# Kernel tuning notes

Measured on AMD Instinct MI355X. Metric: run time of the kernel, lower is better.

Reference implementation:

```python
import math
import jax, jax.numpy as jnp
import numpy as np

NUM_HEADS = 12
KEEP_RATE = 0.7


def setup_inputs() -> dict:
    key = jax.random.key(0)
    k1, k2, k3 = jax.random.split(key, 3)
    B, N, C = 16, 577, 768
    x = jax.random.normal(k1, (B, N, C), dtype=jnp.float32)
    qkv_w = jax.random.normal(k2, (3 * C, C), dtype=jnp.float32) * 0.02
    proj_w = jax.random.normal(k3, (C, C), dtype=jnp.float32) * 0.02
    proj_b = jnp.zeros((C,), dtype=jnp.float32)
    return {"x": x, "qkv_w": qkv_w, "proj_w": proj_w, "proj_b": proj_b}


def reference(x, qkv_w, proj_w, proj_b):
    B, N, C = x.shape
    H = NUM_HEADS
    hd = C // H
    scale = hd ** -0.5
    # qkv projection (no bias): [B, N, 3C] -> [3, B, H, N, hd]
    qkv = (x @ qkv_w.T).reshape(B, N, 3, H, hd).transpose(2, 0, 3, 1, 4)
    q, k, v = qkv[0], qkv[1], qkv[2]
    attn = jax.nn.softmax(jnp.einsum('bhnd,bhmd->bhnm', q, k) * scale, axis=-1)
    out = jnp.einsum('bhnm,bhmd->bhnd', attn, v)          # [B,H,N,hd]
    out = out.transpose(0, 2, 1, 3).reshape(B, N, C)
    out = out @ proj_w.T + proj_b
    # CLS-token attention pruning (keep_rate < 1.0, return_idx=True path)
    left_tokens = math.ceil(KEEP_RATE * (N - 1))
    cls_attn = attn[:, :, 0, 1:].mean(axis=1)             # [B, N-1], mean over heads
    _, idx = jax.lax.top_k(cls_attn, left_tokens)         # sorted descending
    index = jnp.broadcast_to(idx[:, :, None], (B, left_tokens, C))
    return out, idx, index, cls_attn
```

## Files before the change

### kernel.cpp

```cpp
#include <hip/hip_runtime.h>
#include <math.h>

#define BB 16
#define NN 577
#define CC 768
#define HH 12
#define HD 64
#define MM (BB*NN)
#define MPAD 9344
#define LEFT 404
#define NPAD 608
#define NQT 10

typedef __attribute__((ext_vector_type(8))) short short8v;
typedef __attribute__((ext_vector_type(4))) float f32x4;

__device__ __forceinline__ unsigned short f2bf(float f) {
    union { float f; unsigned int u; } v; v.f = f;
    unsigned int r = v.u + 0x7fffu + ((v.u >> 16) & 1u);
    return (unsigned short)(r >> 16);
}

__global__ __launch_bounds__(256) void k_qv_fused(const float* __restrict__ X,
                                                  const float* __restrict__ W,
                                                  float* __restrict__ kb,
                                                  unsigned short* __restrict__ kbh,
                                                  const unsigned short* __restrict__ xbh,
                                                  const unsigned short* __restrict__ wqkv,
                                                  unsigned short* __restrict__ qbh,
                                                  unsigned short* __restrict__ Vt)
{
    __shared__ __align__(16) char smem[16384];
    const int bid = blockIdx.x;
    const int t = threadIdx.x;

    if (bid % 3 == 0) {
        const int kidx = bid / 3;
        float (*Xs)[128] = (float(*)[128])smem;
        float (*Ws)[128] = (float(*)[128])(smem + 8192);
        const int tx = t & 15, ty = t >> 4;
        const int m0 = (kidx % 73) * 128;
        const int n0 = 768 + (kidx / 73) * 128;
        const int sm = t & 127;
        const int sk = (t >> 7) * 8;

        float acc[8][8];
        #pragma unroll
        for (int i = 0; i < 8; ++i)
            #pragma unroll
            for (int j = 0; j < 8; ++j) acc[i][j] = 0.f;

        const int gm = m0 + sm;
        const float* px = X + (size_t)gm * CC + sk;
        const float* pw = W + (size_t)(n0 + sm) * CC + sk;

        float4 a0 = make_float4(0.f,0.f,0.f,0.f), a1 = a0, b0, b1;
        if (gm < MM) { a0 = *(const float4*)px; a1 = *(const float4*)(px + 4); }
        b0 = *(const float4*)pw; b1 = *(const float4*)(pw + 4);

        for (int kk = 0; kk < CC; kk += 16) {
            Xs[sk+0][sm] = a0.x; Xs[sk+1][sm] = a0.y; Xs[sk+2][sm] = a0.z; Xs[sk+3][sm] = a0.w;
            Xs[sk+4][sm] = a1.x; Xs[sk+5][sm] = a1.y; Xs[sk+6][sm] = a1.z; Xs[sk+7][sm] = a1.w;
            Ws[sk+0][sm] = b0.x; Ws[sk+1][sm] = b0.y; Ws[sk+2][sm] = b0.z; Ws[sk+3][sm] = b0.w;
            Ws[sk+4][sm] = b1.x; Ws[sk+5][sm] = b1.y; Ws[sk+6][sm] = b1.z; Ws[sk+7][sm] = b1.w;
            __syncthreads();
            if (kk + 16 < CC) {
                a0 = make_float4(0.f,0.f,0.f,0.f); a1 = a0;
                if (gm < MM) { a0 = *(const float4*)(px + kk + 16); a1 = *(const float4*)(px + kk + 20); }
                b0 = *(const float4*)(pw + kk + 16); b1 = *(const float4*)(pw + kk + 20);
            }
            #pragma unroll
            for (int k = 0; k < 16; ++k) {
                float a[8], bv[8];
                *(float4*)&a[0]  = *(const float4*)&Xs[k][ty*4];
                *(float4*)&a[4]  = *(const float4*)&Xs[k][64 + ty*4];
                *(float4*)&bv[0] = *(const float4*)&Ws[k][tx*4];
                *(float4*)&bv[4] = *(const float4*)&Ws[k][64 + tx*4];
                #pragma unroll
                for (int i = 0; i < 8; ++i)
                    #pragma unroll
                    for (int j = 0; j < 8; ++j)
                        acc[i][j] = fmaf(a[i], bv[j], acc[i][j]);
            }
            __syncthreads();
        }
        #pragma unroll
        for (int i = 0; i < 8; ++i) {
            const int mrow = m0 + ((i < 4) ? (ty*4 + i) : (64 + ty*4 + i - 4));
            if (mrow >= MM) continue;
            const int b_ = mrow / NN;
            const int n_ = mrow - b_ * NN;
            #pragma unroll
            for (int j = 0; j < 8; ++j) {
                const int col = (n0 - 768) + ((j < 4) ? (tx*4 + j) : (64 + tx*4 + j - 4));
                const int h = col >> 6, d = col & 63;
                const float a = acc[i][j];
                kb [(((size_t)b_ * HH + h) * NN   + n_) * HD + d] = a;
                kbh[(((size_t)b_ * HH + h) * NPAD + n_) * HD + d] = f2bf(a);
            }
        }
    } else {
        const int qbid = (bid / 3) * 2 + (bid % 3) - 1;
        unsigned short* As = (unsigned short*)smem;
        unsigned short* Bs = (unsigned short*)(smem + 8192);
        const int w = t >> 6, l = t & 63;
        const int l15 = l & 15, lk = l >> 4;
        const int wm = w >> 1, wn = w & 1;
        const int m0 = (qbid % 73) * 128;
        const int by = qbid / 73;
        const int isV = by >= 6;
        const int nlocal0 = (isV ? (by - 6) : by) * 128;
        const int wrow0 = (isV ? 1536 : 0) + nlocal0;
        const int r0 = t >> 2, segp = t & 3;

        f32x4 acc[4][4];
        #pragma unroll
        for (int i = 0; i < 4; ++i)
            #pragma unroll
            for (int j = 0; j < 4; ++j) acc[i][j] = (f32x4){0.f,0.f,0.f,0.f};

        const unsigned short* ga = xbh  + (size_t)(m0 + r0) * CC + segp * 8;
        const unsigned short* gb = wqkv + (size_t)(wrow0 + r0) * CC + segp * 8;

        for (int kk = 0; kk < CC; kk += 32) {
            const short8v a0 = *(const short8v*)(ga + kk);
            const short8v a1 = *(const short8v*)(ga + kk + (size_t)64 * CC);
            const short8v b0 = *(const short8v*)(gb + kk);
            const short8v b1 = *(const short8v*)(gb + kk + (size_t)64 * CC);
            __syncthreads();
            *(short8v*)&As[(r0)      * 32 + segp*8] = a0;
            *(short8v*)&As[(64 + r0) * 32 + segp*8] = a1;
            *(short8v*)&Bs[(r0)      * 32 + segp*8] = b0;
            *(short8v*)&Bs[(64 + r0) * 32 + segp*8] = b1;
            __syncthreads();
            short8v fa[4], fb[4];
            #pragma unroll
            for (int i = 0; i < 4; ++i) fa[i] = *(const short8v*)&As[(wm*64 + i*16 + l15)*32 + lk*8];
            #pragma unroll
            for (int j = 0; j < 4; ++j) fb[j] = *(const short8v*)&Bs[(wn*64 + j*16 + l15)*32 + lk*8];
            #pragma unroll
            for (int i = 0; i < 4; ++i)
                #pragma unroll
                for (int j = 0; j < 4; ++j)
                    acc[i][j] = __builtin_amdgcn_mfma_f32_16x16x32_bf16(fa[i], fb[j], acc[i][j], 0, 0, 0);
        }

        const int nb = nlocal0 + wn*64 + l15;
        #pragma unroll
        for (int i = 0; i < 4; ++i) {
            #pragma unroll
            for (int r = 0; r < 4; ++r) {
                const int m = m0 + wm*64 + i*16 + 4*lk + r;
                if (m >= MM) continue;
                const int b_ = m / NN, tok = m - b_ * NN;
                #pragma unroll
                for (int j = 0; j < 4; ++j) {
                    const int nl = nb + j*16;
                    const int h = nl >> 6, d = nl & 63;
                    const unsigned short v = f2bf(acc[i][j][r]);
                    if (isV) Vt [(((size_t)b_*HH + h)*HD + d)*NPAD + tok] = v;
                    else     qbh[(((size_t)b_*HH + h)*NPAD + tok)*HD + d] = v;
                }
            }
        }
    }
}

__global__ __launch_bounds__(256) void qcls_kernel(const float* __restrict__ X,
                                                   const float* __restrict__ W,
                                                   float* __restrict__ qcls)
{
    const int b = blockIdx.x;
    const int col = blockIdx.y * 256 + threadIdx.x;
    const float* xr = X + (size_t)b * NN * CC;
    const float* wr = W + (size_t)col * CC;
    float acc = 0.f;
    for (int k = 0; k < CC; ++k) acc = fmaf(xr[k], wr[k], acc);
    qcls[(size_t)b * CC + col] = acc;
}

#define N4X 1772544
#define N4W 442368
#define N4P 147456
__global__ __launch_bounds__(256) void convert3(const float* __restrict__ x,
                                                const float* __restrict__ wq,
                                                const float* __restrict__ wp,
                                                unsigned short* __restrict__ xb,
                                                unsigned short* __restrict__ wqb,
                                                unsigned short* __restrict__ wpb)
{
    int g = blockIdx.x * 256 + threadIdx.x;
    const float* src; unsigned short* dst;
    if (g < N4X)            { src = x;  dst = xb;  }
    else if (g < N4X + N4W) { g -= N4X; src = wq; dst = wqb; }
    else                    { g -= (N4X + N4W); src = wp; dst = wpb; }
    const float4 v = ((const float4*)src)[g];
    ushort4 o;
    o.x = f2bf(v.x); o.y = f2bf(v.y); o.z = f2bf(v.z); o.w = f2bf(v.w);
    ((ushort4*)dst)[g] = o;
}

__global__ __launch_bounds__(256) void proj_mfma(const unsigned short* __restrict__ aobh,
                                                 const unsigned short* __restrict__ wpb,
                                                 const float* __restrict__ bias,
                                                 float* __restrict__ outp)
{
    __shared__ unsigned short As[128*32];
    __shared__ unsigned short Bs[128*32];
    const int t = threadIdx.x;
    const int w = t >> 6, l = t & 63;
    const int l15 = l & 15, lk = l >> 4;
    const int wm = w >> 1, wn = w & 1;
    const int m0 = blockIdx.x * 128;
    const int n0 = blockIdx.y * 128;
    const int r0 = t >> 2, segp = t & 3;

    f32x4 acc[4][4];
    #pragma unroll
    for (int i = 0; i < 4; ++i)
        #pragma unroll
        for (int j = 0; j < 4; ++j) acc[i][j] = (f32x4){0.f,0.f,0.f,0.f};

    const unsigned short* ga = aobh + (size_t)(m0 + r0) * CC + segp * 8;
    const unsigned short* gb = wpb  + (size_t)(n0 + r0) * CC + segp * 8;

    for (int kk = 0; kk < CC; kk += 32) {
        const short8v a0 = *(const short8v*)(ga + kk);
        const short8v a1 = *(const short8v*)(ga + kk + (size_t)64 * CC);
        const short8v b0 = *(const short8v*)(gb + kk);
        const short8v b1 = *(const short8v*)(gb + kk + (size_t)64 * CC);
        __syncthreads();
        *(short8v*)&As[(r0)      * 32 + segp*8] = a0;
        *(short8v*)&As[(64 + r0) * 32 + segp*8] = a1;
        *(short8v*)&Bs[(r0)      * 32 + segp*8] = b0;
        *(short8v*)&Bs[(64 + r0) * 32 + segp*8] = b1;
        __syncthreads();
        short8v fa[4], fb[4];
        #pragma unroll
        for (int i = 0; i < 4; ++i) fa[i] = *(const short8v*)&As[(wm*64 + i*16 + l15)*32 + lk*8];
        #pragma unroll
        for (int j = 0; j < 4; ++j) fb[j] = *(const short8v*)&Bs[(wn*64 + j*16 + l15)*32 + lk*8];
        #pragma unroll
        for (int i = 0; i < 4; ++i)
            #pragma unroll
            for (int j = 0; j < 4; ++j)
                acc[i][j] = __builtin_amdgcn_mfma_f32_16x16x32_bf16(fa[i], fb[j], acc[i][j], 0, 0, 0);
    }

    const int nb = n0 + wn*64 + l15;
    #pragma unroll
    for (int i = 0; i < 4; ++i) {
        #pragma unroll
        for (int r = 0; r < 4; ++r) {
            const int m = m0 + wm*64 + i*16 + 4*lk + r;
            if (m >= MM) continue;
            #pragma unroll
            for (int j = 0; j < 4; ++j) {
                const int n = nb + j*16;
                outp[(size_t)m * CC + n] = acc[i][j][r] + bias[n];
            }
        }
    }
}

__global__ __launch_bounds__(256) void attn_mfma(const unsigned short* __restrict__ qbh,
                                                 const unsigned short* __restrict__ kbh,
                                                 const unsigned short* __restrict__ Vt,
                                                 unsigned short* __restrict__ aobh)
{
    __shared__ __align__(16) unsigned short plds[4][16][32];
    const int bid = blockIdx.x;
    const int bh  = bid / NQT;
    const int qt  = bid - bh * NQT;
    const int b   = bh / HH, h = bh - b * HH;
    const int t   = threadIdx.x;
    const int w   = t >> 6, l = t & 63;
    const int l15 = l & 15, lg = l >> 4;

    short8v aq0, aq1;
    {
        int qrow = qt*64 + w*16 + l15; if (qrow > 576) qrow = 576;
        const unsigned short* qp = qbh + ((size_t)bh * NPAD + qrow) * HD + lg*8;
        aq0 = *(const short8v*)(qp);
        aq1 = *(const short8v*)(qp + 32);
    }

    f32x4 O0 = {0.f,0.f,0.f,0.f}, O1 = O0, O2 = O0, O3 = O0;
    float mr[4] = {-1e30f,-1e30f,-1e30f,-1e30f};
    float lr[4] = {0.f,0.f,0.f,0.f};

    const unsigned short* kwb = kbh + (size_t)bh * NPAD * HD + (size_t)l15 * HD + lg*8;
    const unsigned short* vwb = Vt  + (size_t)bh * HD * NPAD + (size_t)l15 * NPAD + lg*8;

    for (int c = 0; c < 19; ++c) {
        const int n0 = c * 32;
        const unsigned short* kp = kwb + (size_t)n0 * HD;
        short8v bk00 = *(const short8v*)(kp);
        short8v bk01 = *(const short8v*)(kp + 32);
        short8v bk10 = *(const short8v*)(kp + 16*HD);
        short8v bk11 = *(const short8v*)(kp + 16*HD + 32);
        f32x4 s0 = {0.f,0.f,0.f,0.f}, s1 = {0.f,0.f,0.f,0.f};
        s0 = __builtin_amdgcn_mfma_f32_16x16x32_bf16(aq0, bk00, s0, 0, 0, 0);
        s0 = __builtin_amdgcn_mfma_f32_16x16x32_bf16(aq1, bk01, s0, 0, 0, 0);
        s1 = __builtin_amdgcn_mfma_f32_16x16x32_bf16(aq0, bk10, s1, 0, 0, 0);
        s1 = __builtin_amdgcn_mfma_f32_16x16x32_bf16(aq1, bk11, s1, 0, 0, 0);

        const int nc0 = n0 + l15;
        float p0[4], p1[4], al[4];
        #pragma unroll
        for (int r = 0; r < 4; ++r) {
            float a0 = (nc0      <= 576) ? s0[r] * 0.125f : -1e30f;
            float a1 = (nc0 + 16 <= 576) ? s1[r] * 0.125f : -1e30f;
            float tm = fmaxf(a0, a1);
            tm = fmaxf(tm, __shfl_xor(tm, 1, 64));
            tm = fmaxf(tm, __shfl_xor(tm, 2, 64));
            tm = fmaxf(tm, __shfl_xor(tm, 4, 64));
            tm = fmaxf(tm, __shfl_xor(tm, 8, 64));
            const float mn = fmaxf(mr[r], tm);
            al[r] = __expf(mr[r] - mn);
            mr[r] = mn;
            p0[r] = __expf(a0 - mn);
            p1[r] = __expf(a1 - mn);
            float ps = p0[r] + p1[r];
            ps += __shfl_xor(ps, 1, 64);
            ps += __shfl_xor(ps, 2, 64);
            ps += __shfl_xor(ps, 4, 64);
            ps += __shfl_xor(ps, 8, 64);
            lr[r] = lr[r] * al[r] + ps;
        }
        #pragma unroll
        for (int r = 0; r < 4; ++r) {
            O0[r] *= al[r]; O1[r] *= al[r]; O2[r] *= al[r]; O3[r] *= al[r];
        }
        #pragma unroll
        for (int r = 0; r < 4; ++r) {
            plds[w][lg*4 + r][l15]      = f2bf(p0[r]);
            plds[w][lg*4 + r][16 + l15] = f2bf(p1[r]);
        }
        asm volatile("s_waitcnt lgkmcnt(0)" ::: "memory");
        short8v pa = *(const short8v*)&plds[w][l15][lg*8];
        const unsigned short* vp = vwb + n0;
        short8v v0 = *(const short8v*)(vp);
        short8v v1 = *(const short8v*)(vp + 16*NPAD);
        short8v v2 = *(const short8v*)(vp + 32*NPAD);
        short8v v3 = *(const short8v*)(vp + 48*NPAD);
        O0 = __builtin_amdgcn_mfma_f32_16x16x32_bf16(pa, v0, O0, 0, 0, 0);
        O1 = __builtin_amdgcn_mfma_f32_16x16x32_bf16(pa, v1, O1, 0, 0, 0);
        O2 = __builtin_amdgcn_mfma_f32_16x16x32_bf16(pa, v2, O2, 0, 0, 0);
        O3 = __builtin_amdgcn_mfma_f32_16x16x32_bf16(pa, v3, O3, 0, 0, 0);
    }

    #pragma unroll
    for (int r = 0; r < 4; ++r) {
        const float inv = 1.f / lr[r];
        const int row = qt*64 + w*16 + lg*4 + r;
        if (row <= 576) {
            unsigned short* op = aobh + ((size_t)b * NN + row) * CC + h*HD + l15;
            op[0]  = f2bf(O0[r] * inv);
            op[16] = f2bf(O1[r] * inv);
            op[32] = f2bf(O2[r] * inv);
            op[48] = f2bf(O3[r] * inv);
        }
    }
}

__global__ __launch_bounds__(256) void cls_scores(const float* __restrict__ qcls,
                                                  const float* __restrict__ kb,
                                                  float* __restrict__ P)
{
    const int bh = blockIdx.x;
    const int t = threadIdx.x;
    __shared__ float q[64];
    __shared__ float red[256];
    __shared__ float L[NN];
    if (t < 64) q[t] = qcls[(size_t)bh * 64 + t];
    __syncthreads();
    float lmax = -1e30f;
    for (int n = t; n < NN; n += 256) {
        const float* kr = kb + ((size_t)bh * NN + n) * HD;
        float acc = 0.f;
        #pragma unroll
        for (int d = 0; d < 64; ++d) acc = fmaf(q[d], kr[d], acc);
        const float l = acc * 0.125f;
        L[n] = l;
        lmax = fmaxf(lmax, l);
    }
    red[t] = lmax; __syncthreads();
    for (int s = 128; s > 0; s >>= 1) { if (t < s) red[t] = fmaxf(red[t], red[t+s]); __syncthreads(); }
    const float m = red[0]; __syncthreads();
    float z = 0.f;
    for (int n = t; n < NN; n += 256) { const float e = expf(L[n] - m); L[n] = e; z += e; }
    red[t] = z; __syncthreads();
    for (int s = 128; s > 0; s >>= 1) { if (t < s) red[t] += red[t+s]; __syncthreads(); }
    const float Z = red[0];
    for (int n = t; n < NN; n += 256) P[(size_t)bh * NN + n] = L[n] / Z;
}

__global__ __launch_bounds__(256) void cls_mean32(const float* __restrict__ P,
                                                  float* __restrict__ cls32,
                                                  float* __restrict__ out_cls)
{
    const int b = blockIdx.x;
    for (int j = threadIdx.x; j < NN - 1; j += 256) {
        float s = 0.f;
        #pragma unroll
        for (int h = 0; h < HH; ++h) s += P[((size_t)(b * HH + h)) * NN + 1 + j];
        const float v = s / 12.0f;
        cls32[b * 576 + j] = v;
        out_cls[b * 576 + j] = v;
    }
}

__global__ __launch_bounds__(256) void topk_rank(const float* __restrict__ cls32,
                                                 float* __restrict__ out_idx,
                                                 int* __restrict__ idxi)
{
    const int b = blockIdx.x;
    const int t = threadIdx.x;
    __shared__ float sv[576];
    for (int i = t; i < 576; i += 256) sv[i] = cls32[b * 576 + i];
    __syncthreads();
    for (int i = t; i < 576; i += 256) {
        const float vi = sv[i];
        int rank = 0;
        for (int j = 0; j < 576; ++j) {
            const float vj = sv[j];
            if (vj > vi || (vj == vi && j < i)) ++rank;
        }
        if (rank < LEFT) {
            out_idx[(size_t)b * LEFT + rank] = (float)i;
            idxi[(size_t)b * LEFT + rank] = i;
        }
    }
}

__global__ void write_index(const int* __restrict__ idxi, float* __restrict__ out_index)
{
    const int g4 = blockIdx.x * 256 + threadIdx.x;
    const float v = (float)idxi[g4 / 192];
    float4 o; o.x = v; o.y = v; o.z = v; o.w = v;
    ((float4*)out_index)[g4] = o;
}

extern "C" void kernel_launch(void* const* d_in, const int* in_sizes, int n_in,
                              void* d_out, int out_size, void* d_ws, size_t ws_size,
                              hipStream_t stream)
{
    const float* x      = (const float*)d_in[0];
    const float* qkv_w  = (const float*)d_in[1];
    const float* proj_w = (const float*)d_in[2];
    const float* proj_b = (const float*)d_in[3];
    float* out = (float*)d_out;

    char* base = (char*)d_ws;
    float*          kb    = (float*)(base + 0);
    unsigned short* xbh   = (unsigned short*)(base +  28360704);
    unsigned short* qbh   = (unsigned short*)(base +  42713088);
    unsigned short* kbh   = (unsigned short*)(base +  57655296);
    unsigned short* Vt    = (unsigned short*)(base +  72597504);
    unsigned short* aobh  = (unsigned short*)(base +  87539712);
    unsigned short* wqkv  = (unsigned short*)(base + 101892096);
    unsigned short* wpb   = (unsigned short*)(base + 105431040);
    float*          qcls  = (float*)(base + 106610688);
    float*          P     = (float*)(base + 106659840);
    float*          cls32 = (float*)(base + 107102976);
    int*            idxi  = (int*)  (base + 107139840);

    float* out_main  = out;
    float* out_idx   = out + 7090176;
    float* out_index = out + 7096640;
    float* out_cls   = out + 12060992;

    convert3<<<9228, 256, 0, stream>>>(x, qkv_w, proj_w, xbh, wqkv, wpb);
    qcls_kernel<<<dim3(16, 3), 256, 0, stream>>>(x, qkv_w, qcls);
    k_qv_fused<<<1314, 256, 0, stream>>>(x, qkv_w, kb, kbh, xbh, wqkv, qbh, Vt);
    attn_mfma<<<BB * HH * NQT, 256, 0, stream>>>(qbh, kbh, Vt, aobh);
    proj_mfma<<<dim3(73, 6), 256, 0, stream>>>(aobh, wpb, proj_b, out_main);

    cls_scores<<<BB * HH, 256, 0, stream>>>(qcls, kb, P);
    cls_mean32<<<BB, 256, 0, stream>>>(P, cls32, out_cls);
    topk_rank<<<BB, 256, 0, stream>>>(cls32, out_idx, idxi);
    write_index<<<4848, 256, 0, stream>>>(idxi, out_index);
}
```

Baseline: 511.5 us.

## Fuse x bf16 conversion into QV MFMA GEMM, split fused kernel, merge mean+topk

Drops the separate fp32-to-bf16 conversion of x and converts x on the fly inside the Q/V MFMA GEMM's global load path. The previously interleaved K-fp32/QV-MFMA kernel is split back into two separate launches. The cls-mean and top-k rank kernels are merged so the head-mean lives in shared memory. This removes a full bf16 copy of x and an intermediate buffer, but the QV GEMM now reads twice as many bytes of x per tile, and the K GEMM no longer runs alongside the QV blocks in the same launch.

```diff
diff --git a/kernel.cpp b/kernel.cpp
--- a/kernel.cpp
+++ b/kernel.cpp
@@ -21,147 +21,80 @@
     return (unsigned short)(r >> 16);
 }
 
-__global__ __launch_bounds__(256) void k_qv_fused(const float* __restrict__ X,
-                                                  const float* __restrict__ W,
-                                                  float* __restrict__ kb,
-                                                  unsigned short* __restrict__ kbh,
-                                                  const unsigned short* __restrict__ xbh,
-                                                  const unsigned short* __restrict__ wqkv,
-                                                  unsigned short* __restrict__ qbh,
-                                                  unsigned short* __restrict__ Vt)
-{
-    __shared__ __align__(16) char smem[16384];
-    const int bid = blockIdx.x;
-    const int t = threadIdx.x;
-
-    if (bid % 3 == 0) {
-        const int kidx = bid / 3;
-        float (*Xs)[128] = (float(*)[128])smem;
-        float (*Ws)[128] = (float(*)[128])(smem + 8192);
-        const int tx = t & 15, ty = t >> 4;
-        const int m0 = (kidx % 73) * 128;
-        const int n0 = 768 + (kidx / 73) * 128;
-        const int sm = t & 127;
-        const int sk = (t >> 7) * 8;
-
-        float acc[8][8];
-        #pragma unroll
-        for (int i = 0; i < 8; ++i)
+__device__ __forceinline__ short8v cvt8(float4 lo, float4 hi) {
+    short8v r;
+    r[0]=(short)f2bf(lo.x); r[1]=(short)f2bf(lo.y); r[2]=(short)f2bf(lo.z); r[3]=(short)f2bf(lo.w);
+    r[4]=(short)f2bf(hi.x); r[5]=(short)f2bf(hi.y); r[6]=(short)f2bf(hi.z); r[7]=(short)f2bf(hi.w);
+    return r;
+}
+
+__global__ __launch_bounds__(256) void k_gemm_fp32(const float* __restrict__ X,
+                                                   const float* __restrict__ W,
+                                                   float* __restrict__ kb,
+                                                   unsigned short* __restrict__ kbh)
+{
+    __shared__ float Xs[16][128];
+    __shared__ float Ws[16][128];
+    const int t  = threadIdx.x;
+    const int tx = t & 15, ty = t >> 4;
+    const int m0 = blockIdx.x * 128;
+    const int n0 = 768 + blockIdx.y * 128;
+    const int sm = t & 127;
+    const int sk = (t >> 7) * 8;
+
+    float acc[8][8];
+    #pragma unroll
+    for (int i = 0; i < 8; ++i)
+        #pragma unroll
+        for (int j = 0; j < 8; ++j) acc[i][j] = 0.f;
+
+    const int gm = m0 + sm;
+    const float* px = X + (size_t)gm * CC + sk;
+    const float* pw = W + (size_t)(n0 + sm) * CC + sk;
+
+    float4 a0 = make_float4(0.f,0.f,0.f,0.f), a1 = a0, b0, b1;
+    if (gm < MM) { a0 = *(const float4*)px; a1 = *(const float4*)(px + 4); }
+    b0 = *(const float4*)pw; b1 = *(const float4*)(pw + 4);
+
+    for (int kk = 0; kk < CC; kk += 16) {
+        Xs[sk+0][sm] = a0.x; Xs[sk+1][sm] = a0.y; Xs[sk+2][sm] = a0.z; Xs[sk+3][sm] = a0.w;
+        Xs[sk+4][sm] = a1.x; Xs[sk+5][sm] = a1.y; Xs[sk+6][sm] = a1.z; Xs[sk+7][sm] = a1.w;
+        Ws[sk+0][sm] = b0.x; Ws[sk+1][sm] = b0.y; Ws[sk+2][sm] = b0.z; Ws[sk+3][sm] = b0.w;
+        Ws[sk+4][sm] = b1.x; Ws[sk+5][sm] = b1.y; Ws[sk+6][sm] = b1.z; Ws[sk+7][sm] = b1.w;
+        __syncthreads();
+        if (kk + 16 < CC) {
+            a0 = make_float4(0.f,0.f,0.f,0.f); a1 = a0;
+            if (gm < MM) { a0 = *(const float4*)(px + kk + 16); a1 = *(const float4*)(px + kk + 20); }
+            b0 = *(const float4*)(pw + kk + 16); b1 = *(const float4*)(pw + kk + 20);
+        }
+        #pragma unroll
+        for (int k = 0; k < 16; ++k) {
+            float a[8], bv[8];
+            *(float4*)&a[0]  = *(const float4*)&Xs[k][ty*4];
+            *(float4*)&a[4]  = *(const float4*)&Xs[k][64 + ty*4];
+            *(float4*)&bv[0] = *(const float4*)&Ws[k][tx*4];
+            *(float4*)&bv[4] = *(const float4*)&Ws[k][64 + tx*4];
             #pragma unroll
-            for (int j = 0; j < 8; ++j) acc[i][j] = 0.f;
-
-        const int gm = m0 + sm;
-        const float* px = X + (size_t)gm * CC + sk;
-        const float* pw = W + (size_t)(n0 + sm) * CC + sk;
-
-        float4 a0 = make_float4(0.f,0.f,0.f,0.f), a1 = a0, b0, b1;
-        if (gm < MM) { a0 = *(const float4*)px; a1 = *(const float4*)(px + 4); }
-        b0 = *(const float4*)pw; b1 = *(const float4*)(pw + 4);
-
-        for (int kk = 0; kk < CC; kk += 16) {
-            Xs[sk+0][sm] = a0.x; Xs[sk+1][sm] = a0.y; Xs[sk+2][sm] = a0.z; Xs[sk+3][sm] = a0.w;
-            Xs[sk+4][sm] = a1.x; Xs[sk+5][sm] = a1.y; Xs[sk+6][sm] = a1.z; Xs[sk+7][sm] = a1.w;
-            Ws[sk+0][sm] = b0.x; Ws[sk+1][sm] = b0.y; Ws[sk+2][sm] = b0.z; Ws[sk+3][sm] = b0.w;
-            Ws[sk+4][sm] = b1.x; Ws[sk+5][sm] = b1.y; Ws[sk+6][sm] = b1.z; Ws[sk+7][sm] = b1.w;
-            __syncthreads();
-            if (kk + 16 < CC) {
-                a0 = make_float4(0.f,0.f,0.f,0.f); a1 = a0;
-                if (gm < MM) { a0 = *(const float4*)(px + kk + 16); a1 = *(const float4*)(px + kk + 20); }
-                b0 = *(const float4*)(pw + kk + 16); b1 = *(const float4*)(pw + kk + 20);
-            }
-            #pragma unroll
-            for (int k = 0; k < 16; ++k) {
-                float a[8], bv[8];
-                *(float4*)&a[0]  = *(const float4*)&Xs[k][ty*4];
-                *(float4*)&a[4]  = *(const float4*)&Xs[k][64 + ty*4];
-                *(float4*)&bv[0] = *(const float4*)&Ws[k][tx*4];
-                *(float4*)&bv[4] = *(const float4*)&Ws[k][64 + tx*4];
+            for (int i = 0; i < 8; ++i)
                 #pragma unroll
-                for (int i = 0; i < 8; ++i)
-                    #pragma unroll
-                    for (int j = 0; j < 8; ++j)
-                        acc[i][j] = fmaf(a[i], bv[j], acc[i][j]);
-            }
-            __syncthreads();
-        }
-        #pragma unroll
-        for (int i = 0; i < 8; ++i) {
-            const int mrow = m0 + ((i < 4) ? (ty*4 + i) : (64 + ty*4 + i - 4));
-            if (mrow >= MM) continue;
-            const int b_ = mrow / NN;
-            const int n_ = mrow - b_ * NN;
-            #pragma unroll
-            for (int j = 0; j < 8; ++j) {
-                const int col = (n0 - 768) + ((j < 4) ? (tx*4 + j) : (64 + tx*4 + j - 4));
-                const int h = col >> 6, d = col & 63;
-                const float a = acc[i][j];
-                kb [(((size_t)b_ * HH + h) * NN   + n_) * HD + d] = a;
-                kbh[(((size_t)b_ * HH + h) * NPAD + n_) * HD + d] = f2bf(a);
-            }
-        }
-    } else {
-        const int qbid = (bid / 3) * 2 + (bid % 3) - 1;
-        unsigned short* As = (unsigned short*)smem;
-        unsigned short* Bs = (unsigned short*)(smem + 8192);
-        const int w = t >> 6, l = t & 63;
-        const int l15 = l & 15, lk = l >> 4;
-        const int wm = w >> 1, wn = w & 1;
-        const int m0 = (qbid % 73) * 128;
-        const int by = qbid / 73;
-        const int isV = by >= 6;
-        const int nlocal0 = (isV ? (by - 6) : by) * 128;
-        const int wrow0 = (isV ? 1536 : 0) + nlocal0;
-        const int r0 = t >> 2, segp = t & 3;
-
-        f32x4 acc[4][4];
-        #pragma unroll
-        for (int i = 0; i < 4; ++i)
-            #pragma unroll
-            for (int j = 0; j < 4; ++j) acc[i][j] = (f32x4){0.f,0.f,0.f,0.f};
-
-        const unsigned short* ga = xbh  + (size_t)(m0 + r0) * CC + segp * 8;
-        const unsigned short* gb = wqkv + (size_t)(wrow0 + r0) * CC + segp * 8;
-
-        for (int kk = 0; kk < CC; kk += 32) {
-            const short8v a0 = *(const short8v*)(ga + kk);
-            const short8v a1 = *(const short8v*)(ga + kk + (size_t)64 * CC);
-            const short8v b0 = *(const short8v*)(gb + kk);
-            const short8v b1 = *(const short8v*)(gb + kk + (size_t)64 * CC);
-            __syncthreads();
-            *(short8v*)&As[(r0)      * 32 + segp*8] = a0;
-            *(short8v*)&As[(64 + r0) * 32 + segp*8] = a1;
-            *(short8v*)&Bs[(r0)      * 32 + segp*8] = b0;
-            *(short8v*)&Bs[(64 + r0) * 32 + segp*8] = b1;
-            __syncthreads();
-            short8v fa[4], fb[4];
-            #pragma unroll
-            for (int i = 0; i < 4; ++i) fa[i] = *(const short8v*)&As[(wm*64 + i*16 + l15)*32 + lk*8];
-            #pragma unroll
-            for (int j = 0; j < 4; ++j) fb[j] = *(const short8v*)&Bs[(wn*64 + j*16 + l15)*32 + lk*8];
-            #pragma unroll
-            for (int i = 0; i < 4; ++i)
-                #pragma unroll
-                for (int j = 0; j < 4; ++j)
-                    acc[i][j] = __builtin_amdgcn_mfma_f32_16x16x32_bf16(fa[i], fb[j], acc[i][j], 0, 0, 0);
-        }
-
-        const int nb = nlocal0 + wn*64 + l15;
-        #pragma unroll
-        for (int i = 0; i < 4; ++i) {
-            #pragma unroll
-            for (int r = 0; r < 4; ++r) {
-                const int m = m0 + wm*64 + i*16 + 4*lk + r;
-                if (m >= MM) continue;
-                const int b_ = m / NN, tok = m - b_ * NN;
-                #pragma unroll
-                for (int j = 0; j < 4; ++j) {
-                    const int nl = nb + j*16;
-                    const int h = nl >> 6, d = nl & 63;
-                    const unsigned short v = f2bf(acc[i][j][r]);
-                    if (isV) Vt [(((size_t)b_*HH + h)*HD + d)*NPAD + tok] = v;
-                    else     qbh[(((size_t)b_*HH + h)*NPAD + tok)*HD + d] = v;
-                }
-            }
+                for (int j = 0; j < 8; ++j)
+                    acc[i][j] = fmaf(a[i], bv[j], acc[i][j]);
+        }
+        __syncthreads();
+    }
+    #pragma unroll
+    for (int i = 0; i < 8; ++i) {
+        const int mrow = m0 + ((i < 4) ? (ty*4 + i) : (64 + ty*4 + i - 4));
+        if (mrow >= MM) continue;
+        const int b_ = mrow / NN;
+        const int n_ = mrow - b_ * NN;
+        #pragma unroll
+        for (int j = 0; j < 8; ++j) {
+            const int col = (n0 - 768) + ((j < 4) ? (tx*4 + j) : (64 + tx*4 + j - 4));
+            const int h = col >> 6, d = col & 63;
+            const float a = acc[i][j];
+            kb [(((size_t)b_ * HH + h) * NN   + n_) * HD + d] = a;
+            kbh[(((size_t)b_ * HH + h) * NPAD + n_) * HD + d] = f2bf(a);
         }
     }
 }
@@ -179,25 +112,97 @@
     qcls[(size_t)b * CC + col] = acc;
 }
 
-#define N4X 1772544
 #define N4W 442368
 #define N4P 147456
-__global__ __launch_bounds__(256) void convert3(const float* __restrict__ x,
-                                                const float* __restrict__ wq,
-                                                const float* __restrict__ wp,
-                                                unsigned short* __restrict__ xb,
-                                                unsigned short* __restrict__ wqb,
-                                                unsigned short* __restrict__ wpb)
+__global__ __launch_bounds__(256) void convert_w(const float* __restrict__ wq,
+                                                 const float* __restrict__ wp,
+                                                 unsigned short* __restrict__ wqb,
+                                                 unsigned short* __restrict__ wpb)
 {
     int g = blockIdx.x * 256 + threadIdx.x;
     const float* src; unsigned short* dst;
-    if (g < N4X)            { src = x;  dst = xb;  }
-    else if (g < N4X + N4W) { g -= N4X; src = wq; dst = wqb; }
-    else                    { g -= (N4X + N4W); src = wp; dst = wpb; }
+    if (g < N4W)            { src = wq; dst = wqb; }
+    else                    { g -= N4W; src = wp; dst = wpb; }
     const float4 v = ((const float4*)src)[g];
     ushort4 o;
     o.x = f2bf(v.x); o.y = f2bf(v.y); o.z = f2bf(v.z); o.w = f2bf(v.w);
     ((ushort4*)dst)[g] = o;
+}
+
+__global__ __launch_bounds__(256) void qv_mfma(const float* __restrict__ X,
+                                               const unsigned short* __restrict__ wqkv,
+                                               unsigned short* __restrict__ qbh,
+                                               unsigned short* __restrict__ Vt)
+{
+    __shared__ unsigned short As[128*32];
+    __shared__ unsigned short Bs[128*32];
+    const int t = threadIdx.x;
+    const int w = t >> 6, l = t & 63;
+    const int l15 = l & 15, lk = l >> 4;
+    const int wm = w >> 1, wn = w & 1;
+    const int m0 = blockIdx.x * 128;
+    const int isV = blockIdx.y >= 6;
+    const int nlocal0 = (isV ? (blockIdx.y - 6) : blockIdx.y) * 128;
+    const int wrow0 = (isV ? 1536 : 0) + nlocal0;
+    const int r0 = t >> 2, segp = t & 3;
+
+    f32x4 acc[4][4];
+    #pragma unroll
+    for (int i = 0; i < 4; ++i)
+        #pragma unroll
+        for (int j = 0; j < 4; ++j) acc[i][j] = (f32x4){0.f,0.f,0.f,0.f};
+
+    const int gr0 = (m0 + r0      < MM) ? (m0 + r0)      : 0;
+    const int gr1 = (m0 + 64 + r0 < MM) ? (m0 + 64 + r0) : 0;
+    const float* ga0 = X + (size_t)gr0 * CC + segp * 8;
+    const float* ga1 = X + (size_t)gr1 * CC + segp * 8;
+    const unsigned short* gb = wqkv + (size_t)(wrow0 + r0) * CC + segp * 8;
+
+    for (int kk = 0; kk < CC; kk += 32) {
+        const float4 f00 = *(const float4*)(ga0 + kk);
+        const float4 f01 = *(const float4*)(ga0 + kk + 4);
+        const float4 f10 = *(const float4*)(ga1 + kk);
+        const float4 f11 = *(const float4*)(ga1 + kk + 4);
+        const short8v b0 = *(const short8v*)(gb + kk);
+        const short8v b1 = *(const short8v*)(gb + kk + (size_t)64 * CC);
+        const short8v a0 = cvt8(f00, f01);
+        const short8v a1 = cvt8(f10, f11);
+        __syncthreads();
+        *(short8v*)&As[(r0)      * 32 + segp*8] = a0;
+        *(short8v*)&As[(64 + r0) * 32 + segp*8] = a1;
+        *(short8v*)&Bs[(r0)      * 32 + segp*8] = b0;
+        *(short8v*)&Bs[(64 + r0) * 32 + segp*8] = b1;
+        __syncthreads();
+        short8v fa[4], fb[4];
+        #pragma unroll
+        for (int i = 0; i < 4; ++i) fa[i] = *(const short8v*)&As[(wm*64 + i*16 + l15)*32 + lk*8];
+        #pragma unroll
+        for (int j = 0; j < 4; ++j) fb[j] = *(const short8v*)&Bs[(wn*64 + j*16 + l15)*32 + lk*8];
+        #pragma unroll
+        for (int i = 0; i < 4; ++i)
+            #pragma unroll
+            for (int j = 0; j < 4; ++j)
+                acc[i][j] = __builtin_amdgcn_mfma_f32_16x16x32_bf16(fa[i], fb[j], acc[i][j], 0, 0, 0);
+    }
+
+    const int nb = nlocal0 + wn*64 + l15;
+    #pragma unroll
+    for (int i = 0; i < 4; ++i) {
+        #pragma unroll
+        for (int r = 0; r < 4; ++r) {
+            const int m = m0 + wm*64 + i*16 + 4*lk + r;
+            if (m >= MM) continue;
+            const int b_ = m / NN, tok = m - b_ * NN;
+            #pragma unroll
+            for (int j = 0; j < 4; ++j) {
+                const int nl = nb + j*16;
+                const int h = nl >> 6, d = nl & 63;
+                const unsigned short v = f2bf(acc[i][j][r]);
+                if (isV) Vt [(((size_t)b_*HH + h)*HD + d)*NPAD + tok] = v;
+                else     qbh[(((size_t)b_*HH + h)*NPAD + tok)*HD + d] = v;
+            }
+        }
+    }
 }
 
 __global__ __launch_bounds__(256) void proj_mfma(const unsigned short* __restrict__ aobh,
@@ -396,29 +401,22 @@
     for (int n = t; n < NN; n += 256) P[(size_t)bh * NN + n] = L[n] / Z;
 }
 
-__global__ __launch_bounds__(256) void cls_mean32(const float* __restrict__ P,
-                                                  float* __restrict__ cls32,
-                                                  float* __restrict__ out_cls)
-{
-    const int b = blockIdx.x;
-    for (int j = threadIdx.x; j < NN - 1; j += 256) {
-        float s = 0.f;
-        #pragma unroll
-        for (int h = 0; h < HH; ++h) s += P[((size_t)(b * HH + h)) * NN + 1 + j];
-        const float v = s / 12.0f;
-        cls32[b * 576 + j] = v;
-        out_cls[b * 576 + j] = v;
-    }
-}
-
-__global__ __launch_bounds__(256) void topk_rank(const float* __restrict__ cls32,
-                                                 float* __restrict__ out_idx,
-                                                 int* __restrict__ idxi)
+__global__ __launch_bounds__(256) void cls_meantopk(const float* __restrict__ P,
+                                                    float* __restrict__ out_cls,
+                                                    float* __restrict__ out_idx,
+                                                    int* __restrict__ idxi)
 {
     const int b = blockIdx.x;
     const int t = threadIdx.x;
     __shared__ float sv[576];
-    for (int i = t; i < 576; i += 256) sv[i] = cls32[b * 576 + i];
+    for (int j = t; j < 576; j += 256) {
+        float s = 0.f;
+        #pragma unroll
+        for (int h = 0; h < HH; ++h) s += P[((size_t)(b * HH + h)) * NN + 1 + j];
+        const float v = s / 12.0f;
+        sv[j] = v;
+        out_cls[b * 576 + j] = v;
+    }
     __syncthreads();
     for (int i = t; i < 576; i += 256) {
         const float vi = sv[i];
@@ -454,7 +452,6 @@
 
     char* base = (char*)d_ws;
     float*          kb    = (float*)(base + 0);
-    unsigned short* xbh   = (unsigned short*)(base +  28360704);
     unsigned short* qbh   = (unsigned short*)(base +  42713088);
     unsigned short* kbh   = (unsigned short*)(base +  57655296);
     unsigned short* Vt    = (unsigned short*)(base +  72597504);
@@ -463,7 +460,6 @@
     unsigned short* wpb   = (unsigned short*)(base + 105431040);
     float*          qcls  = (float*)(base + 106610688);
     float*          P     = (float*)(base + 106659840);
-    float*          cls32 = (float*)(base + 107102976);
     int*            idxi  = (int*)  (base + 107139840);
 
     float* out_main  = out;
@@ -471,14 +467,14 @@
     float* out_index = out + 7096640;
     float* out_cls   = out + 12060992;
 
-    convert3<<<9228, 256, 0, stream>>>(x, qkv_w, proj_w, xbh, wqkv, wpb);
+    convert_w<<<2304, 256, 0, stream>>>(qkv_w, proj_w, wqkv, wpb);
     qcls_kernel<<<dim3(16, 3), 256, 0, stream>>>(x, qkv_w, qcls);
-    k_qv_fused<<<1314, 256, 0, stream>>>(x, qkv_w, kb, kbh, xbh, wqkv, qbh, Vt);
+    k_gemm_fp32<<<dim3(73, 6), 256, 0, stream>>>(x, qkv_w, kb, kbh);
+    qv_mfma<<<dim3(73, 12), 256, 0, stream>>>(x, wqkv, qbh, Vt);
     attn_mfma<<<BB * HH * NQT, 256, 0, stream>>>(qbh, kbh, Vt, aobh);
     proj_mfma<<<dim3(73, 6), 256, 0, stream>>>(aobh, wpb, proj_b, out_main);
 
     cls_scores<<<BB * HH, 256, 0, stream>>>(qcls, kb, P);
-    cls_mean32<<<BB, 256, 0, stream>>>(P, cls32, out_cls);
-    topk_rank<<<BB, 256, 0, stream>>>(cls32, out_idx, idxi);
+    cls_meantopk<<<BB, 256, 0, stream>>>(P, out_cls, out_idx, idxi);
     write_index<<<4848, 256, 0, stream>>>(idxi, out_index);
 }
```

Result: faster. 452.4 us (-11.5%).
